# Optimization experiments

Hardware: AMD Instinct MI355X
Metric: run time of the kernel (lower is better)

## Reference

```python
import jax, jax.numpy as jnp
import numpy as np

E, H, V, B, T = 256, 512, 50257, 4, 512
EPS = 1e-5  # torch F.layer_norm default


def _ln(x):
    m = jnp.mean(x, axis=-1, keepdims=True)
    v = jnp.var(x, axis=-1, keepdims=True)
    return (x - m) / jnp.sqrt(v + EPS)


def setup_inputs() -> dict:
    key = jax.random.key(0)
    ks = iter(jax.random.split(key, 40))

    def w(shape):
        return jax.random.normal(next(ks), shape, dtype=jnp.float32) * 0.02

    inp = {"input_ids": jax.random.randint(next(ks), (B, T), 0, V)}
    inp["emb_table"] = w((V, E))
    for i, e in [(0, E), (1, H)]:  # layer 0 input = emb_dim, layer 1 input = hidden_dim
        inp[f"Wc1_{i}"] = w((2 * H + e, 2 * H)); inp[f"bc1_{i}"] = w((2 * H,))
        inp[f"Wc2_{i}"] = w((2 * H, H));         inp[f"bc2_{i}"] = w((H,))
        inp[f"Wg1_{i}"] = w((2 * H + e, H));     inp[f"bg1_{i}"] = w((H,))
        inp[f"Wg2_{i}"] = w((H, 1));             inp[f"bg2_{i}"] = w((1,))
        inp[f"Wr_{i}"] = w((e, H));              inp[f"br_{i}"] = w((H,))
    inp["Wa1"] = w((H, H)); inp["ba1"] = w((H,))
    inp["Wa2"] = w((H, 1)); inp["ba2"] = w((1,))
    inp["Wh"] = w((H, V));  inp["bh"] = w((V,))
    return inp


def _forward(input_ids, emb_table,
             Wc1_0, bc1_0, Wc2_0, bc2_0, Wg1_0, bg1_0, Wg2_0, bg2_0, Wr_0, br_0,
             Wc1_1, bc1_1, Wc2_1, bc2_1, Wg1_1, bg1_1, Wg2_1, bg2_1, Wr_1, br_1,
             Wa1, ba1, Wa2, ba2, Wh, bh):
    layers = [
        (Wc1_0, bc1_0, Wc2_0, bc2_0, Wg1_0, bg1_0, Wg2_0, bg2_0, Wr_0, br_0),
        (Wc1_1, bc1_1, Wc2_1, bc2_1, Wg1_1, bg1_1, Wg2_1, bg2_1, Wr_1, br_1),
    ]
    emb = emb_table[input_ids]  # [B,T,E]

    def step(carry, x_t):
        h2s, h1s = carry  # tuples of [B,H] per layer
        new_h2, new_h1 = [], []
        inp = x_t
        gate = None
        for (Wc1, bc1, Wc2, bc2, Wg1, bg1, Wg2, bg2, Wr, br), h2, h1 in zip(layers, h2s, h1s):
            ctx = jnp.concatenate([h1, h2, inp], axis=-1)  # [B, 2H+e]
            cand = jnp.maximum(ctx @ Wc1 + bc1, 0.0) @ Wc2 + bc2
            gate = jax.nn.sigmoid(jnp.tanh(ctx @ Wg1 + bg1) @ Wg2 + bg2)[:, 0]  # [B]
            h = _ln(h1 + gate[:, None] * cand + 0.1 * (inp @ Wr + br))
            new_h2.append(h1); new_h1.append(h)
            inp = h
        return (tuple(new_h2), tuple(new_h1)), (inp, gate)

    z = jnp.zeros((B, H), emb.dtype)
    init = ((z, z), (z, z))
    _, (hist, gates) = jax.lax.scan(step, init, jnp.swapaxes(emb, 0, 1))
    hist = jnp.swapaxes(hist, 0, 1)    # [B,T,H] last-layer hidden states
    gates = jnp.swapaxes(gates, 0, 1)  # [B,T]

    # Additive attention over the growing prefix: scores are fixed per position,
    # so prefix-softmax context = cumsum(exp(s)*h) / cumsum(exp(s)).
    scores = (jnp.tanh(hist @ Wa1 + ba1) @ Wa2 + ba2)[..., 0]  # [B,T]
    m = jnp.max(scores, axis=1, keepdims=True)
    e = jnp.exp(scores - m)
    num = jnp.cumsum(e[..., None] * hist, axis=1)  # [B,T,H]
    den = jnp.cumsum(e, axis=1)[..., None]
    attended = hist + num / den
    logits = attended @ Wh + bh  # [B,T,V]
    return logits, gates


def reference(input_ids, emb_table,
              Wc1_0, bc1_0, Wc2_0, bc2_0, Wg1_0, bg1_0, Wg2_0, bg2_0, Wr_0, br_0,
              Wc1_1, bc1_1, Wc2_1, bc2_1, Wg1_1, bg1_1, Wg2_1, bg2_1, Wr_1, br_1,
              Wa1, ba1, Wa2, ba2, Wh, bh):
    return _forward(input_ids, emb_table,
                    Wc1_0, bc1_0, Wc2_0, bc2_0, Wg1_0, bg1_0, Wg2_0, bg2_0, Wr_0, br_0,
                    Wc1_1, bc1_1, Wc2_1, bc2_1, Wg1_1, bg1_1, Wg2_1, bg2_1, Wr_1, br_1,
                    Wa1, ba1, Wa2, ba2, Wh, bh)
```

## Files before the change

### kernel.cpp

```cpp
#include <hip/hip_runtime.h>
#include <hip/hip_fp16.h>
#include <cstdint>
#include <cstddef>

typedef unsigned short u16;
typedef unsigned int   u32;
typedef unsigned long long u64;

#define Bn 4
#define Tn 512
#define Hn 512
#define En 256
#define Vn 50257
#define NPAD 50304
#define RG  256
#define RNT 256

typedef _Float16 h2t __attribute__((ext_vector_type(2)));

#if defined(__has_builtin)
#if __has_builtin(__builtin_amdgcn_fdot2)
#define HAS_FDOT2 1
#endif
#endif
__device__ __forceinline__ float fdot2f(h2t a, h2t b, float c) {
#ifdef HAS_FDOT2
  return __builtin_amdgcn_fdot2(a, b, c, false);
#else
  return fmaf((float)a[0], (float)b[0], fmaf((float)a[1], (float)b[1], c));
#endif
}

__device__ __forceinline__ u16 f2bf(float f) {
  u32 x; __builtin_memcpy(&x, &f, 4);
  u32 r = (x + 0x7fffu + ((x >> 16) & 1u)) >> 16;
  return (u16)r;
}
__device__ __forceinline__ u16 f2h(float f) {
  __half hh = __float2half(f); u16 u; __builtin_memcpy(&u, &hh, 2); return u;
}
__device__ __forceinline__ u64 gldu64(const u64* p) {
  return __hip_atomic_load(p, __ATOMIC_RELAXED, __HIP_MEMORY_SCOPE_AGENT);
}
__device__ __forceinline__ void gstu64(u64* p, u64 v) {
  __hip_atomic_store(p, v, __ATOMIC_RELAXED, __HIP_MEMORY_SCOPE_AGENT);
}
__device__ __forceinline__ u32 gldu32(const u32* p) {
  return __hip_atomic_load(p, __ATOMIC_RELAXED, __HIP_MEMORY_SCOPE_AGENT);
}
__device__ __forceinline__ void gstu32(u32* p, u32 v) {
  __hip_atomic_store(p, v, __ATOMIC_RELAXED, __HIP_MEMORY_SCOPE_AGENT);
}
__device__ __forceinline__ void gstf(float* p, float v) {
  __hip_atomic_store(p, v, __ATOMIC_RELAXED, __HIP_MEMORY_SCOPE_AGENT);
}

__global__ __launch_bounds__(256) void transpose_h(
    const float* __restrict__ src, __half* __restrict__ dst, int K, int N)
{
  __shared__ float tile[32][33];
  const int tx = threadIdx.x & 31, ty = threadIdx.x >> 5;
  const int bn = blockIdx.x * 32, bk = blockIdx.y * 32;
  #pragma unroll
  for (int i = 0; i < 4; ++i)
    tile[ty + i * 8][tx] = src[(size_t)(bk + ty + i * 8) * N + bn + tx];
  __syncthreads();
  #pragma unroll
  for (int i = 0; i < 4; ++i)
    dst[(size_t)(bn + ty + i * 8) * K + bk + tx] = __float2half(tile[tx][ty + i * 8]);
}

__global__ __launch_bounds__(256) void convwh_kernel(
    const float* __restrict__ wh, u16* __restrict__ whb)
{
  const int k = blockIdx.y;
  const int v0 = (blockIdx.x * 256 + threadIdx.x) * 2;
  if (v0 >= NPAD) return;
  float a = (v0     < Vn) ? wh[(size_t)k * Vn + v0]     : 0.f;
  float b = (v0 + 1 < Vn) ? wh[(size_t)k * Vn + v0 + 1] : 0.f;
  u32 pack = (u32)f2bf(a) | ((u32)f2bf(b) << 16);
  *(u32*)&whb[(size_t)k * NPAD + v0] = pack;
}

#define HR16_B  98304
#define HR0_B   102400
#define EMB_B   104448
#define XCAND_B 105472
#define GP_B    109568
#define RLOC_B  110080
#define SS_B    110144
#define BC1L_B  110464
#define BG1L_B  110528
#define BC2L_B  110560
#define BRL_B   110592
#define WG2L_B  110624
#define BG2L_B  110656
#define STW_B   110720
#define STW0_B  110784
#define REC_LDS 110848

__global__ __launch_bounds__(RNT, 1) void rec_kernel(
    const int* __restrict__ ids, const float* __restrict__ emb,
    const __half* wtC1_0, const __half* wtG1_0, const __half* wtC2_0, const __half* wtR_0,
    const __half* wtC1_1, const __half* wtG1_1, const __half* wtC2_1, const __half* wtR_1,
    const float* bc1_0, const float* bg1_0, const float* bc2_0, const float* br_0,
    const float* wg2_0, const float* bg2_0,
    const float* bc1_1, const float* bg1_1, const float* bc2_1, const float* br_1,
    const float* wg2_1, const float* bg2_1,
    u32* flagA, u64* HB, u64* CB,
    float* __restrict__ histN, float* __restrict__ gates_out)
{
  extern __shared__ char smem[];
  __half* WL    = (__half*)smem;
  __half* hr16  = (__half*)(smem + HR16_B);
  __half* hr0   = (__half*)(smem + HR0_B);
  __half* xcand = (__half*)(smem + XCAND_B);
  float* gp     = (float*)(smem + GP_B);
  float* rloc   = (float*)(smem + RLOC_B);
  float* Ss     = (float*)(smem + SS_B);
  float* bc1L   = (float*)(smem + BC1L_B);
  float* bg1L   = (float*)(smem + BG1L_B);
  float* bc2L   = (float*)(smem + BC2L_B);
  float* brL    = (float*)(smem + BRL_B);
  float* wg2L   = (float*)(smem + WG2L_B);
  float* bg2L   = (float*)(smem + BG2L_B);
  float* stw    = (float*)(smem + STW_B);
  float* stw0   = (float*)(smem + STW0_B);

  const int tid = threadIdx.x, g = blockIdx.x;
  const int bp = g >> 7, l = (g >> 6) & 1, gl = g & 63;
  const int w = tid >> 6, lane = tid & 63;
  const int C = l ? 1536 : 1280;
  const int e = l ? 512 : 256;
  const int oG1 = 16 * C, oR = 24 * C, oC2 = 24 * C + 8 * e;

  const __half* wtC1 = l ? wtC1_1 : wtC1_0;
  const __half* wtG1 = l ? wtG1_1 : wtG1_0;
  const __half* wtC2 = l ? wtC2_1 : wtC2_0;
  const __half* wtR  = l ? wtR_1  : wtR_0;
  const float* bc1 = l ? bc1_1 : bc1_0;
  const float* bg1 = l ? bg1_1 : bg1_0;
  const float* bc2 = l ? bc2_1 : bc2_0;
  const float* br  = l ? br_1  : br_0;
  const float* wg2 = l ? wg2_1 : wg2_0;
  const float* bg2 = l ? bg2_1 : bg2_0;

  u64* HBown = HB + (size_t)((bp * 2 + l) * 2) * 512;
  u64* CBown = CB + (size_t)((bp * 2 + l) * 2) * 1152;
  const u64* HBl0 = HB + (size_t)((bp * 2) * 2) * 512;

  {
    auto cp = [&](const __half* src, int nh, int offh) {
      const u32* s = (const u32*)src; u32* d = (u32*)(WL + offh);
      for (int i = tid; i < (nh >> 1); i += RNT) d[i] = s[i];
    };
    cp(wtC1 + (size_t)(gl * 16) * C, 16 * C, 0);
    cp(wtG1 + (size_t)(gl * 8) * C,  8 * C, oG1);
    cp(wtR  + (size_t)(gl * 8) * e,  8 * e, oR);
    cp(wtC2 + (size_t)(gl * 8) * 1024, 8 * 1024, oC2);
  }
  for (int i = tid; i < 2960; i += RNT) ((u32*)(smem + HR16_B))[i] = 0;
  __syncthreads();

  if (tid < 16)      bc1L[tid] = bc1[gl * 16 + tid];
  else if (tid < 24) bg1L[tid - 16] = bg1[gl * 8 + tid - 16];
  else if (tid < 32) bc2L[tid - 24] = bc2[gl * 8 + tid - 24];
  else if (tid < 40) brL[tid - 32]  = br[gl * 8 + tid - 32];
  else if (tid < 48) wg2L[tid - 40] = wg2[gl * 8 + tid - 40];
  else if (tid == 48) bg2L[0] = bg2[0];
  for (int task = w; task < 32; task += 4) {
    const __half* colp; int K;
    if (task < 16)      { colp = WL + (size_t)task * C;              K = C; }
    else if (task < 24) { colp = WL + oG1 + (size_t)(task - 16) * C; K = C; }
    else                { colp = WL + oR  + (size_t)(task - 24) * e; K = e; }
    float s1 = 0.f, s2 = 0.f, s3 = 0.f;
    for (int k = lane; k < K; k += 64) {
      float v = __half2float(colp[k]);
      if (K == e) s1 += v;
      else if (k < 512) s1 += v;
      else if (k < 1024) s2 += v;
      else s3 += v;
    }
    #pragma unroll
    for (int off = 32; off; off >>= 1) {
      s1 += __shfl_xor(s1, off); s2 += __shfl_xor(s2, off); s3 += __shfl_xor(s3, off);
    }
    if (lane == 0) {
      if (task < 16)      { Ss[task] = s1; Ss[16 + task] = s2; Ss[32 + task] = s3; }
      else if (task < 24) { Ss[48 + task - 16] = s1; Ss[56 + task - 16] = s2; Ss[64 + task - 16] = s3; }
      else                { Ss[72 + task - 24] = s1; }
    }
  }
  __syncthreads();

  const int nEnd = l ? (Tn + 1) : (Tn - 1);
  float mp[2] = {0.f, 0.f}, ipv[2] = {0.f, 0.f};

  for (int n = 0; n <= nEnd; ++n) {
    const int t = n - l;
    const bool prod = (t >= 0) && (t < Tn);
    const bool pollOwn = (t >= 1) && (t <= Tn);
    const bool pollL0  = (l == 1) && prod;
    const int parR = (n - 1) & 1;

    h2t er0[2], er1[2];
    er0[0] = (h2t)0; er0[1] = (h2t)0; er1[0] = (h2t)0; er1[1] = (h2t)0;
    if (l == 0 && prod) {
      int id0 = ids[(bp * 2) * Tn + t];
      int id1 = ids[(bp * 2 + 1) * Tn + t];
      float2 fa0 = *(const float2*)(emb + (size_t)id0 * En + 2 * lane);
      float2 fb0 = *(const float2*)(emb + (size_t)id0 * En + 2 * (lane + 64));
      float2 fa1 = *(const float2*)(emb + (size_t)id1 * En + 2 * lane);
      float2 fb1 = *(const float2*)(emb + (size_t)id1 * En + 2 * (lane + 64));
      er0[0][0] = (_Float16)fa0.x; er0[0][1] = (_Float16)fa0.y;
      er0[1][0] = (_Float16)fb0.x; er0[1][1] = (_Float16)fb0.y;
      er1[0][0] = (_Float16)fa1.x; er1[0][1] = (_Float16)fa1.y;
      er1[1][0] = (_Float16)fb1.x; er1[1][1] = (_Float16)fb1.y;
    }

    float comb[8][2];
    #pragma unroll
    for (int c = 0; c < 8; ++c) { comb[c][0] = 0.f; comb[c][1] = 0.f; }
    if (prod) {
      const __half* h2pl[2] = { hr16 + ((parR ^ 1) * 2) * 512,
                                hr16 + ((parR ^ 1) * 2 + 1) * 512 };
      float a[8][2];
      if (w < 3) {
        const __half* wbase = (w < 2) ? (WL + (size_t)(w * 8) * C) : (WL + oG1);
        #pragma unroll
        for (int c = 0; c < 8; ++c) { a[c][0] = 0.f; a[c][1] = 0.f; }
        #pragma unroll
        for (int it = 0; it < 4; ++it) {
          int p2 = lane + it * 64;
          h2t x0 = *(const h2t*)(h2pl[0] + 2 * p2);
          h2t x1 = *(const h2t*)(h2pl[1] + 2 * p2);
          #pragma unroll
          for (int c = 0; c < 8; ++c) {
            h2t wv = *(const h2t*)(wbase + (size_t)c * C + 512 + 2 * p2);
            a[c][0] = fdot2f(wv, x0, a[c][0]);
            a[c][1] = fdot2f(wv, x1, a[c][1]);
          }
        }
        #pragma unroll
        for (int c = 0; c < 8; ++c) { comb[c][0] += ipv[0] * a[c][0]; comb[c][1] += ipv[1] * a[c][1]; }
        if (l == 0) {
          #pragma unroll
          for (int c = 0; c < 8; ++c) { a[c][0] = 0.f; a[c][1] = 0.f; }
          #pragma unroll
          for (int it = 0; it < 2; ++it) {
            int p2 = lane + it * 64;
            #pragma unroll
            for (int c = 0; c < 8; ++c) {
              h2t wv = *(const h2t*)(wbase + (size_t)c * C + 1024 + 2 * p2);
              a[c][0] = fdot2f(wv, er0[it], a[c][0]);
              a[c][1] = fdot2f(wv, er1[it], a[c][1]);
            }
          }
          #pragma unroll
          for (int c = 0; c < 8; ++c) { comb[c][0] += a[c][0]; comb[c][1] += a[c][1]; }
        }
      } else if (l == 0) {
        #pragma unroll
        for (int c = 0; c < 8; ++c) { a[c][0] = 0.f; a[c][1] = 0.f; }
        #pragma unroll
        for (int it = 0; it < 2; ++it) {
          int p2 = lane + it * 64;
          #pragma unroll
          for (int c = 0; c < 8; ++c) {
            h2t wv = *(const h2t*)(WL + oR + (size_t)c * e + 2 * p2);
            a[c][0] = fdot2f(wv, er0[it], a[c][0]);
            a[c][1] = fdot2f(wv, er1[it], a[c][1]);
          }
        }
        #pragma unroll
        for (int c = 0; c < 8; ++c) { comb[c][0] = a[c][0]; comb[c][1] = a[c][1]; }
      }
    }

    if (pollOwn || pollL0) {
      const u64* s1 = HBown + (size_t)parR * 512;
      const u64* s0 = HBl0 + (size_t)parR * 512;
      const u32 want = (u32)n;
      u64 v1[2], v0[2];
      for (;;) {
        bool ok = true;
        if (pollOwn) { v1[0] = gldu64(s1 + tid); v1[1] = gldu64(s1 + 256 + tid); }
        if (pollL0)  { v0[0] = gldu64(s0 + tid); v0[1] = gldu64(s0 + 256 + tid); }
        if (pollOwn) ok &= ((u32)(v1[0] >> 32) == want) & ((u32)(v1[1] >> 32) == want);
        if (pollL0)  ok &= ((u32)(v0[0] >> 32) == want) & ((u32)(v0[1] >> 32) == want);
        if (ok) break;
        __builtin_amdgcn_s_sleep(2);
      }
      if (pollOwn) {
        float sb0 = 0.f, sb1 = 0.f, qb0 = 0.f, qb1 = 0.f;
        #pragma unroll
        for (int i = 0; i < 2; ++i) {
          int W = i * 256 + tid;
          int glp = W >> 3, q = W & 7, cpp = q >> 1, b = q & 1;
          u32 pay = (u32)v1[i];
          ((u32*)(hr16 + (parR * 2 + b) * 512))[glp * 4 + cpp] = pay;
          __half2 hh; __builtin_memcpy(&hh, &pay, 4);
          float2 fv = __half22float2(hh);
          float sv = fv.x + fv.y, qv = fv.x * fv.x + fv.y * fv.y;
          if (b == 0) { sb0 += sv; qb0 += qv; } else { sb1 += sv; qb1 += qv; }
        }
        #pragma unroll
        for (int off = 32; off; off >>= 1) {
          sb0 += __shfl_xor(sb0, off); qb0 += __shfl_xor(qb0, off);
          sb1 += __shfl_xor(sb1, off); qb1 += __shfl_xor(qb1, off);
        }
        if (lane == 0) { stw[w * 4] = sb0; stw[w * 4 + 1] = sb1; stw[w * 4 + 2] = qb0; stw[w * 4 + 3] = qb1; }
      }
      if (pollL0) {
        float sb0 = 0.f, sb1 = 0.f, qb0 = 0.f, qb1 = 0.f;
        #pragma unroll
        for (int i = 0; i < 2; ++i) {
          int W = i * 256 + tid;
          int glp = W >> 3, q = W & 7, cpp = q >> 1, b = q & 1;
          u32 pay = (u32)v0[i];
          ((u32*)(hr0 + b * 512))[glp * 4 + cpp] = pay;
          __half2 hh; __builtin_memcpy(&hh, &pay, 4);
          float2 fv = __half22float2(hh);
          float sv = fv.x + fv.y, qv = fv.x * fv.x + fv.y * fv.y;
          if (b == 0) { sb0 += sv; qb0 += qv; } else { sb1 += sv; qb1 += qv; }
        }
        #pragma unroll
        for (int off = 32; off; off >>= 1) {
          sb0 += __shfl_xor(sb0, off); qb0 += __shfl_xor(qb0, off);
          sb1 += __shfl_xor(sb1, off); qb1 += __shfl_xor(qb1, off);
        }
        if (lane == 0) { stw0[w * 4] = sb0; stw0[w * 4 + 1] = sb1; stw0[w * 4 + 2] = qb0; stw0[w * 4 + 3] = qb1; }
      }
    }
    __syncthreads();
    if (l == 1 && tid == 0) gstu32(flagA + (bp * 64 + gl) * 16, (u32)(n + 1));

    float m1[2] = {0.f, 0.f}, i1v[2] = {0.f, 0.f};
    float m3[2] = {0.f, 0.f}, i3v[2] = {0.f, 0.f};
    if (pollOwn) {
      float S0 = stw[0] + stw[4] + stw[8] + stw[12];
      float S1 = stw[1] + stw[5] + stw[9] + stw[13];
      float Q0 = stw[2] + stw[6] + stw[10] + stw[14];
      float Q1 = stw[3] + stw[7] + stw[11] + stw[15];
      m1[0] = S0 * (1.f / 512.f); i1v[0] = rsqrtf(Q0 * (1.f / 512.f) - m1[0] * m1[0] + 1e-5f);
      m1[1] = S1 * (1.f / 512.f); i1v[1] = rsqrtf(Q1 * (1.f / 512.f) - m1[1] * m1[1] + 1e-5f);
    }
    if (pollL0) {
      float S0 = stw0[0] + stw0[4] + stw0[8] + stw0[12];
      float S1 = stw0[1] + stw0[5] + stw0[9] + stw0[13];
      float Q0 = stw0[2] + stw0[6] + stw0[10] + stw0[14];
      float Q1 = stw0[3] + stw0[7] + stw0[11] + stw0[15];
      m3[0] = S0 * (1.f / 512.f); i3v[0] = rsqrtf(Q0 * (1.f / 512.f) - m3[0] * m3[0] + 1e-5f);
      m3[1] = S1 * (1.f / 512.f); i3v[1] = rsqrtf(Q1 * (1.f / 512.f) - m3[1] * m3[1] + 1e-5f);
    }

    if (l == 1 && pollOwn && tid < 16) {
      int c = tid >> 1, b = tid & 1, j = gl * 8 + c;
      float rv = __half2float(hr16[(parR * 2 + b) * 512 + j]);
      gstf(histN + ((size_t)((bp * 2 + b) * Tn + (t - 1))) * Hn + j, (rv - m1[b]) * i1v[b]);
    }

    if (prod) {
      const __half* h1pl[2] = { hr16 + (parR * 2) * 512, hr16 + (parR * 2 + 1) * 512 };
      float a[8][2];
      if (w < 3) {
        const __half* wbase = (w < 2) ? (WL + (size_t)(w * 8) * C) : (WL + oG1);
        #pragma unroll
        for (int c = 0; c < 8; ++c) { a[c][0] = 0.f; a[c][1] = 0.f; }
        #pragma unroll
        for (int it = 0; it < 4; ++it) {
          int p2 = lane + it * 64;
          h2t x0 = *(const h2t*)(h1pl[0] + 2 * p2);
          h2t x1 = *(const h2t*)(h1pl[1] + 2 * p2);
          #pragma unroll
          for (int c = 0; c < 8; ++c) {
            h2t wv = *(const h2t*)(wbase + (size_t)c * C + 2 * p2);
            a[c][0] = fdot2f(wv, x0, a[c][0]);
            a[c][1] = fdot2f(wv, x1, a[c][1]);
          }
        }
        #pragma unroll
        for (int c = 0; c < 8; ++c) { comb[c][0] += i1v[0] * a[c][0]; comb[c][1] += i1v[1] * a[c][1]; }
        if (l == 1) {
          #pragma unroll
          for (int c = 0; c < 8; ++c) { a[c][0] = 0.f; a[c][1] = 0.f; }
          #pragma unroll
          for (int it = 0; it < 4; ++it) {
            int p2 = lane + it * 64;
            h2t x0 = *(const h2t*)(hr0 + 2 * p2);
            h2t x1 = *(const h2t*)(hr0 + 512 + 2 * p2);
            #pragma unroll
            for (int c = 0; c < 8; ++c) {
              h2t wv = *(const h2t*)(wbase + (size_t)c * C + 1024 + 2 * p2);
              a[c][0] = fdot2f(wv, x0, a[c][0]);
              a[c][1] = fdot2f(wv, x1, a[c][1]);
            }
          }
          #pragma unroll
          for (int c = 0; c < 8; ++c) { comb[c][0] += i3v[0] * a[c][0]; comb[c][1] += i3v[1] * a[c][1]; }
        }
      } else if (l == 1) {
        #pragma unroll
        for (int c = 0; c < 8; ++c) { a[c][0] = 0.f; a[c][1] = 0.f; }
        #pragma unroll
        for (int it = 0; it < 4; ++it) {
          int p2 = lane + it * 64;
          h2t x0 = *(const h2t*)(hr0 + 2 * p2);
          h2t x1 = *(const h2t*)(hr0 + 512 + 2 * p2);
          #pragma unroll
          for (int c = 0; c < 8; ++c) {
            h2t wv = *(const h2t*)(WL + oR + (size_t)c * e + 2 * p2);
            a[c][0] = fdot2f(wv, x0, a[c][0]);
            a[c][1] = fdot2f(wv, x1, a[c][1]);
          }
        }
        #pragma unroll
        for (int c = 0; c < 8; ++c) { comb[c][0] = i3v[0] * a[c][0]; comb[c][1] = i3v[1] * a[c][1]; }
      }

      #pragma unroll
      for (int off = 32; off; off >>= 1)
        #pragma unroll
        for (int c = 0; c < 8; ++c) {
          comb[c][0] += __shfl_xor(comb[c][0], off);
          comb[c][1] += __shfl_xor(comb[c][1], off);
        }
      float v0s = 0.f, v1s = 0.f;
      #pragma unroll
      for (int c = 0; c < 8; ++c)
        if (lane == c) { v0s = comb[c][0]; v1s = comb[c][1]; }

      const u64 tagw = ((u64)(u32)(n + 1)) << 32;
      u64* CBw = CBown + (size_t)(n & 1) * 1152 + gl * 18;
      if (w < 2) {
        if (lane < 8) {
          int cg = w * 8 + lane;
          float k0 = i1v[0] * m1[0] * Ss[cg] + ipv[0] * mp[0] * Ss[16 + cg];
          float k1 = i1v[1] * m1[1] * Ss[cg] + ipv[1] * mp[1] * Ss[16 + cg];
          if (l) { k0 += i3v[0] * m3[0] * Ss[32 + cg]; k1 += i3v[1] * m3[1] * Ss[32 + cg]; }
          float bb = bc1L[cg];
          float c0 = fmaxf(v0s - k0 + bb, 0.f), c1 = fmaxf(v1s - k1 + bb, 0.f);
          u32 pay = (u32)f2h(c0) | ((u32)f2h(c1) << 16);
          gstu64(CBw + cg, tagw | pay);
        }
      } else if (w == 2) {
        if (lane < 8) {
          float k0 = i1v[0] * m1[0] * Ss[48 + lane] + ipv[0] * mp[0] * Ss[56 + lane];
          float k1 = i1v[1] * m1[1] * Ss[48 + lane] + ipv[1] * mp[1] * Ss[56 + lane];
          if (l) { k0 += i3v[0] * m3[0] * Ss[64 + lane]; k1 += i3v[1] * m3[1] * Ss[64 + lane]; }
          float bgv = bg1L[lane], wgv = wg2L[lane];
          float t0 = tanhf(v0s - k0 + bgv) * wgv;
          float t1 = tanhf(v1s - k1 + bgv) * wgv;
          #pragma unroll
          for (int off = 1; off < 8; off <<= 1) { t0 += __shfl_xor(t0, off); t1 += __shfl_xor(t1, off); }
          if (lane == 0) {
            u32 b0, b1; __builtin_memcpy(&b0, &t0, 4); __builtin_memcpy(&b1, &t1, 4);
            gstu64(CBw + 16, tagw | b0);
            gstu64(CBw + 17, tagw | b1);
          }
        }
      } else {
        if (lane < 8) {
          float k0 = l ? i3v[0] * m3[0] * Ss[72 + lane] : 0.f;
          float k1 = l ? i3v[1] * m3[1] * Ss[72 + lane] : 0.f;
          rloc[lane * 2]     = v0s - k0 + brL[lane];
          rloc[lane * 2 + 1] = v1s - k1 + brL[lane];
        }
      }
    }

    if (prod) {
      const u64* CBL = CBown + (size_t)(n & 1) * 1152;
      const u32 want = (u32)(n + 1);
      const bool needF = (l == 0) && (tid < 64);
      const u32* fptr = flagA + (bp * 64 + tid) * 16;
      u64 cv[5];
      const bool last = (tid < 128);
      for (;;) {
        bool ok = true;
        #pragma unroll
        for (int i = 0; i < 4; ++i) cv[i] = gldu64(CBL + i * 256 + tid);
        if (last) cv[4] = gldu64(CBL + 1024 + tid);
        #pragma unroll
        for (int i = 0; i < 4; ++i) ok &= ((u32)(cv[i] >> 32) == want);
        if (last) ok &= ((u32)(cv[4] >> 32) == want);
        if (needF) ok &= (gldu32(fptr) >= (u32)n);
        if (ok) break;
        __builtin_amdgcn_s_sleep(2);
      }
      u16* xc16 = (u16*)xcand;
      #pragma unroll
      for (int i = 0; i < 5; ++i) {
        if (i == 4 && !last) break;
        int idx = i * 256 + tid;
        int p = (int)(((u32)idx * 3641u) >> 16);
        int w2 = idx - p * 18;
        u32 pay = (u32)cv[i];
        if (w2 < 16) {
          int j = p * 16 + w2;
          xc16[j]        = (u16)(pay & 0xffffu);
          xc16[1024 + j] = (u16)(pay >> 16);
        } else {
          float f; __builtin_memcpy(&f, &pay, 4);
          gp[p * 2 + (w2 - 16)] = f;
        }
      }
    }
    __syncthreads();

    if (prod) {
      float gs0 = gp[lane * 2], gs1 = gp[lane * 2 + 1];
      #pragma unroll
      for (int off = 32; off; off >>= 1) { gs0 += __shfl_xor(gs0, off); gs1 += __shfl_xor(gs1, off); }
      float gate[2];
      gate[0] = 1.f / (1.f + expf(-(gs0 + bg2L[0])));
      gate[1] = 1.f / (1.f + expf(-(gs1 + bg2L[0])));

      float a2[2][2];
      a2[0][0] = a2[0][1] = a2[1][0] = a2[1][1] = 0.f;
      const __half* wb2 = WL + oC2 + (w * 2) * 1024;
      #pragma unroll
      for (int it = 0; it < 8; ++it) {
        int p2 = lane + it * 64;
        h2t xv0 = *(const h2t*)(xcand + 2 * p2);
        h2t xv1 = *(const h2t*)(xcand + 1024 + 2 * p2);
        #pragma unroll
        for (int cc = 0; cc < 2; ++cc) {
          h2t wv = *(const h2t*)(wb2 + cc * 1024 + 2 * p2);
          a2[cc][0] = fdot2f(wv, xv0, a2[cc][0]);
          a2[cc][1] = fdot2f(wv, xv1, a2[cc][1]);
        }
      }
      #pragma unroll
      for (int off = 32; off; off >>= 1)
        #pragma unroll
        for (int cc = 0; cc < 2; ++cc) {
          a2[cc][0] += __shfl_xor(a2[cc][0], off);
          a2[cc][1] += __shfl_xor(a2[cc][1], off);
        }
      float sel = 0.f;
      #pragma unroll
      for (int cc = 0; cc < 2; ++cc)
        #pragma unroll
        for (int b = 0; b < 2; ++b)
          if (lane == cc * 2 + b) sel = a2[cc][b];
      int cc = (lane >> 1) & 1, b = lane & 1, cl = w * 2 + cc;
      float rv = __half2float(hr16[(parR * 2 + b) * 512 + gl * 8 + cl]);
      float h1n = (rv - m1[b]) * i1v[b];
      float hv = h1n + gate[b] * (sel + bc2L[cl]) + 0.1f * rloc[cl * 2 + b];
      float hv0 = __shfl(hv, 0), hv1 = __shfl(hv, 1);
      float hv2 = __shfl(hv, 2), hv3 = __shfl(hv, 3);
      if (lane < 2) {
        u32 pay = (lane == 0) ? ((u32)f2h(hv0) | ((u32)f2h(hv2) << 16))
                              : ((u32)f2h(hv1) | ((u32)f2h(hv3) << 16));
        u64* HBw = HBown + (size_t)(n & 1) * 512 + gl * 8;
        gstu64(HBw + w * 2 + lane, (((u64)(u32)(n + 1)) << 32) | pay);
      }
      if (l == 1 && gl == 0 && w == 0 && lane == 0) {
        gstf(gates_out + (bp * 2) * Tn + t, gate[0]);
        gstf(gates_out + (bp * 2 + 1) * Tn + t, gate[1]);
      }
    }

    if (pollOwn) { mp[0] = m1[0]; mp[1] = m1[1]; ipv[0] = i1v[0]; ipv[1] = i1v[1]; }
  }
}

__global__ __launch_bounds__(256) void scores_kernel(
    const float* __restrict__ histN,
    const float* __restrict__ wa1, const float* __restrict__ ba1,
    const float* __restrict__ wa2, const float* __restrict__ ba2,
    float* __restrict__ scores)
{
  __shared__ float xs[8][512];
  __shared__ float wacc[4][8];
  const int tid = threadIdx.x, bid = blockIdx.x;

  for (int idx = tid; idx < 4096; idx += 256)
    xs[idx >> 9][idx & 511] = histN[(size_t)(bid * 8) * Hn + idx];
  __syncthreads();

  float pr[8] = {0.f,0.f,0.f,0.f,0.f,0.f,0.f,0.f};
  #pragma unroll
  for (int cc = 0; cc < 2; ++cc) {
    int c = tid + cc * 256;
    float a[8] = {0.f,0.f,0.f,0.f,0.f,0.f,0.f,0.f};
    for (int k = 0; k < 512; ++k) {
      float wv = wa1[(size_t)k * 512 + c];
      #pragma unroll
      for (int r = 0; r < 8; ++r) a[r] = fmaf(xs[r][k], wv, a[r]);
    }
    float b1 = ba1[c], w2 = wa2[c];
    #pragma unroll
    for (int r = 0; r < 8; ++r) pr[r] += tanhf(a[r] + b1) * w2;
  }
  int lane = tid & 63, wq = tid >> 6;
  #pragma unroll
  for (int off = 32; off; off >>= 1)
    #pragma unroll
    for (int r = 0; r < 8; ++r) pr[r] += __shfl_xor(pr[r], off);
  if (lane == 0) {
    #pragma unroll
    for (int r = 0; r < 8; ++r) wacc[wq][r] = pr[r];
  }
  __syncthreads();
  if (tid < 8)
    scores[bid * 8 + tid] = wacc[0][tid] + wacc[1][tid] + wacc[2][tid] + wacc[3][tid] + ba2[0];
}

__global__ __launch_bounds__(256) void cumsum_scan_kernel(
    const float* __restrict__ scores, const float* __restrict__ histN,
    u16* __restrict__ att)
{
  __shared__ float ee[512], sa[512], sb[512], red[256];
  __shared__ float tile[64][64];
  const int tid = threadIdx.x;
  const int b = blockIdx.y, j0 = blockIdx.x * 64;

  float s0 = scores[b * Tn + tid], s1 = scores[b * Tn + tid + 256];
  red[tid] = fmaxf(s0, s1);
  __syncthreads();
  for (int s = 128; s; s >>= 1) { if (tid < s) red[tid] = fmaxf(red[tid], red[tid + s]); __syncthreads(); }
  float m = red[0];
  ee[tid] = expf(s0 - m); ee[tid + 256] = expf(s1 - m);
  sa[tid] = ee[tid]; sa[tid + 256] = ee[tid + 256];
  __syncthreads();
  float* A = sa; float* D = sb;
  for (int off = 1; off < 512; off <<= 1) {
    for (int t2 = tid; t2 < 512; t2 += 256) { float v = A[t2]; if (t2 >= off) v += A[t2 - off]; D[t2] = v; }
    __syncthreads();
    float* tmp = A; A = D; D = tmp;
  }
  float* R = D;
  for (int t2 = tid; t2 < 512; t2 += 256) R[t2] = 1.f / A[t2];
  __syncthreads();

  float ax = 0.f;
  for (int tt = 0; tt < 8; ++tt) {
    #pragma unroll
    for (int k = 0; k < 16; ++k) {
      int idx = tid + k * 256;
      int r = idx >> 6, c = idx & 63;
      tile[r][c] = histN[(size_t)(b * Tn + tt * 64 + r) * Hn + j0 + c];
    }
    __syncthreads();
    if (tid < 64) {
      for (int r = 0; r < 64; ++r) {
        int t = tt * 64 + r;
        float x = tile[r][tid];
        ax = fmaf(ee[t], x, ax);
        att[((size_t)(b * Tn + t)) * Hn + j0 + tid] = f2bf(x + ax * R[t]);
      }
    }
    __syncthreads();
  }
}

typedef short bf16x8_t __attribute__((ext_vector_type(8)));
typedef float f32x4_t  __attribute__((ext_vector_type(4)));

__global__ __launch_bounds__(256) void gemm_kernel(
    const u16* __restrict__ Aw, const u16* __restrict__ Bw,
    const float* __restrict__ bh, float* __restrict__ out)
{
  __shared__ u16 Alds[128 * 64];
  __shared__ u16 Blds[64 * 128];
  const int tid = threadIdx.x;
  const int n0 = blockIdx.x * 128, m0 = blockIdx.y * 128;
  const int w = tid >> 6, lane = tid & 63;
  const int wm = (w & 1) * 64, wn = (w >> 1) * 64;

  f32x4_t acc[4][4];
  #pragma unroll
  for (int i = 0; i < 4; ++i)
    #pragma unroll
    for (int j = 0; j < 4; ++j) acc[i][j] = (f32x4_t){0.f, 0.f, 0.f, 0.f};

  for (int kt = 0; kt < 8; ++kt) {
    const int k0 = kt * 64;
    {
      int row = tid >> 1, kc = (tid & 1) * 32;
      #pragma unroll
      for (int jj = 0; jj < 4; ++jj) {
        uint4 v = *(const uint4*)(Aw + (size_t)(m0 + row) * 512 + k0 + kc + jj * 8);
        int byte = row * 128 + (kc + jj * 8) * 2;
        byte ^= (row & 7) << 4;
        *(uint4*)((char*)Alds + byte) = v;
      }
    }
    {
      #pragma unroll
      for (int q = 0; q < 4; ++q) {
        int r = (tid >> 4) + q * 16, c8 = (tid & 15) * 8;
        uint4 v = *(const uint4*)(Bw + (size_t)(k0 + r) * NPAD + n0 + c8);
        *(uint4*)&Blds[r * 128 + c8] = v;
      }
    }
    __syncthreads();
    #pragma unroll
    for (int kh = 0; kh < 2; ++kh) {
      bf16x8_t af[4];
      #pragma unroll
      for (int i = 0; i < 4; ++i) {
        int row = wm + i * 16 + (lane & 15);
        int byte = row * 128 + kh * 64 + (lane >> 4) * 16;
        byte ^= (row & 7) << 4;
        af[i] = *(const bf16x8_t*)((const char*)Alds + byte);
      }
      const int kb = kh * 32 + (lane >> 4) * 8;
      #pragma unroll
      for (int j = 0; j < 4; ++j) {
        int col = wn + j * 16 + (lane & 15);
        bf16x8_t bf;
        #pragma unroll
        for (int jj = 0; jj < 8; ++jj) bf[jj] = (short)Blds[(kb + jj) * 128 + col];
        #pragma unroll
        for (int i = 0; i < 4; ++i)
          acc[i][j] = __builtin_amdgcn_mfma_f32_16x16x32_bf16(af[i], bf, acc[i][j], 0, 0, 0);
      }
    }
    __syncthreads();
  }
  #pragma unroll
  for (int j = 0; j < 4; ++j) {
    int col = n0 + wn + j * 16 + (lane & 15);
    if (col < Vn) {
      float bias = bh[col];
      #pragma unroll
      for (int i = 0; i < 4; ++i) {
        int rbase = m0 + wm + i * 16 + (lane >> 4) * 4;
        #pragma unroll
        for (int r = 0; r < 4; ++r)
          out[(size_t)(rbase + r) * Vn + col] = acc[i][j][r] + bias;
      }
    }
  }
}

extern "C" void kernel_launch(void* const* d_in, const int* in_sizes, int n_in,
                              void* d_out, int out_size, void* d_ws, size_t ws_size,
                              hipStream_t stream) {
  const int*   ids  = (const int*)d_in[0];
  const float* emb  = (const float*)d_in[1];
  const float* Wc1_0 = (const float*)d_in[2];  const float* bc1_0 = (const float*)d_in[3];
  const float* Wc2_0 = (const float*)d_in[4];  const float* bc2_0 = (const float*)d_in[5];
  const float* Wg1_0 = (const float*)d_in[6];  const float* bg1_0 = (const float*)d_in[7];
  const float* Wg2_0 = (const float*)d_in[8];  const float* bg2_0 = (const float*)d_in[9];
  const float* Wr_0  = (const float*)d_in[10]; const float* br_0  = (const float*)d_in[11];
  const float* Wc1_1 = (const float*)d_in[12]; const float* bc1_1 = (const float*)d_in[13];
  const float* Wc2_1 = (const float*)d_in[14]; const float* bc2_1 = (const float*)d_in[15];
  const float* Wg1_1 = (const float*)d_in[16]; const float* bg1_1 = (const float*)d_in[17];
  const float* Wg2_1 = (const float*)d_in[18]; const float* bg2_1 = (const float*)d_in[19];
  const float* Wr_1  = (const float*)d_in[20]; const float* br_1  = (const float*)d_in[21];
  const float* Wa1 = (const float*)d_in[22]; const float* ba1 = (const float*)d_in[23];
  const float* Wa2 = (const float*)d_in[24]; const float* ba2 = (const float*)d_in[25];
  const float* Wh  = (const float*)d_in[26]; const float* bh  = (const float*)d_in[27];

  float* out = (float*)d_out;
  char*  ws  = (char*)d_ws;

  const size_t OFF_FLAGA = 0;
  const size_t OFF_HB    = 8192;
  const size_t OFF_CB    = 40960;
  const size_t OFF_WT    = 114688;
  const size_t OFF_HISTN = OFF_WT + 11534336;
  const size_t OFF_SCO   = OFF_HISTN + 4194304;
  const size_t OFF_ATT   = OFF_SCO + 8192;
  const size_t OFF_WHB   = OFF_ATT + 2097152;

  u32*   flagA  = (u32*)(ws + OFF_FLAGA);
  u64*   HB     = (u64*)(ws + OFF_HB);
  u64*   CB     = (u64*)(ws + OFF_CB);
  __half* wth   = (__half*)(ws + OFF_WT);
  float* histN  = (float*)(ws + OFF_HISTN);
  float* scores = (float*)(ws + OFF_SCO);
  u16*   att    = (u16*)(ws + OFF_ATT);
  u16*   whb    = (u16*)(ws + OFF_WHB);
  float* gates  = out + (size_t)Bn * Tn * Vn;

  __half* wtC1_0h = wth;
  __half* wtG1_0h = wth + 1310720;
  __half* wtC2_0h = wth + 1966080;
  __half* wtR_0h  = wth + 2490368;
  __half* wtC1_1h = wth + 2621440;
  __half* wtG1_1h = wth + 4194304;
  __half* wtC2_1h = wth + 4980736;
  __half* wtR_1h  = wth + 5505024;

  hipMemsetAsync(ws, 0, 114688, stream);

  transpose_h<<<dim3(32, 40), 256, 0, stream>>>(Wc1_0, wtC1_0h, 1280, 1024);
  transpose_h<<<dim3(16, 40), 256, 0, stream>>>(Wg1_0, wtG1_0h, 1280, 512);
  transpose_h<<<dim3(16, 32), 256, 0, stream>>>(Wc2_0, wtC2_0h, 1024, 512);
  transpose_h<<<dim3(16,  8), 256, 0, stream>>>(Wr_0,  wtR_0h,   256, 512);
  transpose_h<<<dim3(32, 48), 256, 0, stream>>>(Wc1_1, wtC1_1h, 1536, 1024);
  transpose_h<<<dim3(16, 48), 256, 0, stream>>>(Wg1_1, wtG1_1h, 1536, 512);
  transpose_h<<<dim3(16, 32), 256, 0, stream>>>(Wc2_1, wtC2_1h, 1024, 512);
  transpose_h<<<dim3(16, 16), 256, 0, stream>>>(Wr_1,  wtR_1h,   512, 512);

  convwh_kernel<<<dim3(99, 512), 256, 0, stream>>>(Wh, whb);

  (void)hipFuncSetAttribute((const void*)rec_kernel,
                            hipFuncAttributeMaxDynamicSharedMemorySize, REC_LDS);

  rec_kernel<<<dim3(RG), dim3(RNT), REC_LDS, stream>>>(
      ids, emb,
      wtC1_0h, wtG1_0h, wtC2_0h, wtR_0h,
      wtC1_1h, wtG1_1h, wtC2_1h, wtR_1h,
      bc1_0, bg1_0, bc2_0, br_0, Wg2_0, bg2_0,
      bc1_1, bg1_1, bc2_1, br_1, Wg2_1, bg2_1,
      flagA, HB, CB, histN, gates);

  scores_kernel<<<dim3(256), 256, 0, stream>>>(histN, Wa1, ba1, Wa2, ba2, scores);

  cumsum_scan_kernel<<<dim3(8, Bn), 256, 0, stream>>>(scores, histN, att);

  gemm_kernel<<<dim3(393, 16), 256, 0, stream>>>(att, whb, bh, out);
}
```

Baseline: 4.331 ms.

## Split polling so layer-1 consumes layer-0 input before waiting on own recurrence

The combined wait for the block's own previous hidden state and layer 0's new output is split into two phases. Layer-1 blocks now poll only for the layer-0 output first, publish their flag, and compute the matvec contributions that depend on it (the input part of the context, plus the residual projection). Only after that do they wait for their own recurrent state and finish the h1 part. This moves work ahead of the longer recurrence dependency to shorten each step's critical path, at the cost of an extra __syncthreads and a reordered comb accumulation that has to stay consistent (the l==0 path now uses += instead of =).

```diff
diff --git a/kernel.cpp b/kernel.cpp
--- a/kernel.cpp
+++ b/kernel.cpp
@@ -273,45 +273,21 @@
           }
         }
         #pragma unroll
-        for (int c = 0; c < 8; ++c) { comb[c][0] = a[c][0]; comb[c][1] = a[c][1]; }
-      }
-    }
-
-    if (pollOwn || pollL0) {
-      const u64* s1 = HBown + (size_t)parR * 512;
-      const u64* s0 = HBl0 + (size_t)parR * 512;
-      const u32 want = (u32)n;
-      u64 v1[2], v0[2];
-      for (;;) {
-        bool ok = true;
-        if (pollOwn) { v1[0] = gldu64(s1 + tid); v1[1] = gldu64(s1 + 256 + tid); }
-        if (pollL0)  { v0[0] = gldu64(s0 + tid); v0[1] = gldu64(s0 + 256 + tid); }
-        if (pollOwn) ok &= ((u32)(v1[0] >> 32) == want) & ((u32)(v1[1] >> 32) == want);
-        if (pollL0)  ok &= ((u32)(v0[0] >> 32) == want) & ((u32)(v0[1] >> 32) == want);
-        if (ok) break;
-        __builtin_amdgcn_s_sleep(2);
-      }
-      if (pollOwn) {
-        float sb0 = 0.f, sb1 = 0.f, qb0 = 0.f, qb1 = 0.f;
-        #pragma unroll
-        for (int i = 0; i < 2; ++i) {
-          int W = i * 256 + tid;
-          int glp = W >> 3, q = W & 7, cpp = q >> 1, b = q & 1;
-          u32 pay = (u32)v1[i];
-          ((u32*)(hr16 + (parR * 2 + b) * 512))[glp * 4 + cpp] = pay;
-          __half2 hh; __builtin_memcpy(&hh, &pay, 4);
-          float2 fv = __half22float2(hh);
-          float sv = fv.x + fv.y, qv = fv.x * fv.x + fv.y * fv.y;
-          if (b == 0) { sb0 += sv; qb0 += qv; } else { sb1 += sv; qb1 += qv; }
-        }
-        #pragma unroll
-        for (int off = 32; off; off >>= 1) {
-          sb0 += __shfl_xor(sb0, off); qb0 += __shfl_xor(qb0, off);
-          sb1 += __shfl_xor(sb1, off); qb1 += __shfl_xor(qb1, off);
-        }
-        if (lane == 0) { stw[w * 4] = sb0; stw[w * 4 + 1] = sb1; stw[w * 4 + 2] = qb0; stw[w * 4 + 3] = qb1; }
-      }
+        for (int c = 0; c < 8; ++c) { comb[c][0] += a[c][0]; comb[c][1] += a[c][1]; }
+      }
+    }
+
+    float m3[2] = {0.f, 0.f}, i3v[2] = {0.f, 0.f};
+    if (l == 1) {
       if (pollL0) {
+        const u64* s0 = HBl0 + (size_t)parR * 512;
+        const u32 want = (u32)n;
+        u64 v0[2];
+        for (;;) {
+          v0[0] = gldu64(s0 + tid); v0[1] = gldu64(s0 + 256 + tid);
+          if (((u32)(v0[0] >> 32) == want) & ((u32)(v0[1] >> 32) == want)) break;
+          __builtin_amdgcn_s_sleep(2);
+        }
         float sb0 = 0.f, sb1 = 0.f, qb0 = 0.f, qb1 = 0.f;
         #pragma unroll
         for (int i = 0; i < 2; ++i) {
@@ -331,59 +307,22 @@
         }
         if (lane == 0) { stw0[w * 4] = sb0; stw0[w * 4 + 1] = sb1; stw0[w * 4 + 2] = qb0; stw0[w * 4 + 3] = qb1; }
       }
-    }
-    __syncthreads();
-    if (l == 1 && tid == 0) gstu32(flagA + (bp * 64 + gl) * 16, (u32)(n + 1));
-
-    float m1[2] = {0.f, 0.f}, i1v[2] = {0.f, 0.f};
-    float m3[2] = {0.f, 0.f}, i3v[2] = {0.f, 0.f};
-    if (pollOwn) {
-      float S0 = stw[0] + stw[4] + stw[8] + stw[12];
-      float S1 = stw[1] + stw[5] + stw[9] + stw[13];
-      float Q0 = stw[2] + stw[6] + stw[10] + stw[14];
-      float Q1 = stw[3] + stw[7] + stw[11] + stw[15];
-      m1[0] = S0 * (1.f / 512.f); i1v[0] = rsqrtf(Q0 * (1.f / 512.f) - m1[0] * m1[0] + 1e-5f);
-      m1[1] = S1 * (1.f / 512.f); i1v[1] = rsqrtf(Q1 * (1.f / 512.f) - m1[1] * m1[1] + 1e-5f);
-    }
-    if (pollL0) {
-      float S0 = stw0[0] + stw0[4] + stw0[8] + stw0[12];
-      float S1 = stw0[1] + stw0[5] + stw0[9] + stw0[13];
-      float Q0 = stw0[2] + stw0[6] + stw0[10] + stw0[14];
-      float Q1 = stw0[3] + stw0[7] + stw0[11] + stw0[15];
-      m3[0] = S0 * (1.f / 512.f); i3v[0] = rsqrtf(Q0 * (1.f / 512.f) - m3[0] * m3[0] + 1e-5f);
-      m3[1] = S1 * (1.f / 512.f); i3v[1] = rsqrtf(Q1 * (1.f / 512.f) - m3[1] * m3[1] + 1e-5f);
-    }
-
-    if (l == 1 && pollOwn && tid < 16) {
-      int c = tid >> 1, b = tid & 1, j = gl * 8 + c;
-      float rv = __half2float(hr16[(parR * 2 + b) * 512 + j]);
-      gstf(histN + ((size_t)((bp * 2 + b) * Tn + (t - 1))) * Hn + j, (rv - m1[b]) * i1v[b]);
-    }
-
-    if (prod) {
-      const __half* h1pl[2] = { hr16 + (parR * 2) * 512, hr16 + (parR * 2 + 1) * 512 };
-      float a[8][2];
-      if (w < 3) {
-        const __half* wbase = (w < 2) ? (WL + (size_t)(w * 8) * C) : (WL + oG1);
+      __syncthreads();
+      if (tid == 0) gstu32(flagA + (bp * 64 + gl) * 16, (u32)(n + 1));
+      if (pollL0) {
+        {
+          float S0 = stw0[0] + stw0[4] + stw0[8] + stw0[12];
+          float S1 = stw0[1] + stw0[5] + stw0[9] + stw0[13];
+          float Q0 = stw0[2] + stw0[6] + stw0[10] + stw0[14];
+          float Q1 = stw0[3] + stw0[7] + stw0[11] + stw0[15];
+          m3[0] = S0 * (1.f / 512.f); i3v[0] = rsqrtf(Q0 * (1.f / 512.f) - m3[0] * m3[0] + 1e-5f);
+          m3[1] = S1 * (1.f / 512.f); i3v[1] = rsqrtf(Q1 * (1.f / 512.f) - m3[1] * m3[1] + 1e-5f);
+        }
+        float a[8][2];
         #pragma unroll
         for (int c = 0; c < 8; ++c) { a[c][0] = 0.f; a[c][1] = 0.f; }
-        #pragma unroll
-        for (int it = 0; it < 4; ++it) {
-          int p2 = lane + it * 64;
-          h2t x0 = *(const h2t*)(h1pl[0] + 2 * p2);
-          h2t x1 = *(const h2t*)(h1pl[1] + 2 * p2);
-          #pragma unroll
-          for (int c = 0; c < 8; ++c) {
-            h2t wv = *(const h2t*)(wbase + (size_t)c * C + 2 * p2);
-            a[c][0] = fdot2f(wv, x0, a[c][0]);
-            a[c][1] = fdot2f(wv, x1, a[c][1]);
-          }
-        }
-        #pragma unroll
-        for (int c = 0; c < 8; ++c) { comb[c][0] += i1v[0] * a[c][0]; comb[c][1] += i1v[1] * a[c][1]; }
-        if (l == 1) {
-          #pragma unroll
-          for (int c = 0; c < 8; ++c) { a[c][0] = 0.f; a[c][1] = 0.f; }
+        if (w < 3) {
+          const __half* wbase = (w < 2) ? (WL + (size_t)(w * 8) * C) : (WL + oG1);
           #pragma unroll
           for (int it = 0; it < 4; ++it) {
             int p2 = lane + it * 64;
@@ -396,26 +335,92 @@
               a[c][1] = fdot2f(wv, x1, a[c][1]);
             }
           }
+        } else {
           #pragma unroll
-          for (int c = 0; c < 8; ++c) { comb[c][0] += i3v[0] * a[c][0]; comb[c][1] += i3v[1] * a[c][1]; }
-        }
-      } else if (l == 1) {
+          for (int it = 0; it < 4; ++it) {
+            int p2 = lane + it * 64;
+            h2t x0 = *(const h2t*)(hr0 + 2 * p2);
+            h2t x1 = *(const h2t*)(hr0 + 512 + 2 * p2);
+            #pragma unroll
+            for (int c = 0; c < 8; ++c) {
+              h2t wv = *(const h2t*)(WL + oR + (size_t)c * e + 2 * p2);
+              a[c][0] = fdot2f(wv, x0, a[c][0]);
+              a[c][1] = fdot2f(wv, x1, a[c][1]);
+            }
+          }
+        }
+        #pragma unroll
+        for (int c = 0; c < 8; ++c) { comb[c][0] += i3v[0] * a[c][0]; comb[c][1] += i3v[1] * a[c][1]; }
+      }
+    }
+
+    if (pollOwn) {
+      const u64* s1 = HBown + (size_t)parR * 512;
+      const u32 want = (u32)n;
+      u64 v1[2];
+      for (;;) {
+        v1[0] = gldu64(s1 + tid); v1[1] = gldu64(s1 + 256 + tid);
+        if (((u32)(v1[0] >> 32) == want) & ((u32)(v1[1] >> 32) == want)) break;
+        __builtin_amdgcn_s_sleep(2);
+      }
+      float sb0 = 0.f, sb1 = 0.f, qb0 = 0.f, qb1 = 0.f;
+      #pragma unroll
+      for (int i = 0; i < 2; ++i) {
+        int W = i * 256 + tid;
+        int glp = W >> 3, q = W & 7, cpp = q >> 1, b = q & 1;
+        u32 pay = (u32)v1[i];
+        ((u32*)(hr16 + (parR * 2 + b) * 512))[glp * 4 + cpp] = pay;
+        __half2 hh; __builtin_memcpy(&hh, &pay, 4);
+        float2 fv = __half22float2(hh);
+        float sv = fv.x + fv.y, qv = fv.x * fv.x + fv.y * fv.y;
+        if (b == 0) { sb0 += sv; qb0 += qv; } else { sb1 += sv; qb1 += qv; }
+      }
+      #pragma unroll
+      for (int off = 32; off; off >>= 1) {
+        sb0 += __shfl_xor(sb0, off); qb0 += __shfl_xor(qb0, off);
+        sb1 += __shfl_xor(sb1, off); qb1 += __shfl_xor(qb1, off);
+      }
+      if (lane == 0) { stw[w * 4] = sb0; stw[w * 4 + 1] = sb1; stw[w * 4 + 2] = qb0; stw[w * 4 + 3] = qb1; }
+    }
+    __syncthreads();
+
+    float m1[2] = {0.f, 0.f}, i1v[2] = {0.f, 0.f};
+    if (pollOwn) {
+      float S0 = stw[0] + stw[4] + stw[8] + stw[12];
+      float S1 = stw[1] + stw[5] + stw[9] + stw[13];
+      float Q0 = stw[2] + stw[6] + stw[10] + stw[14];
+      float Q1 = stw[3] + stw[7] + stw[11] + stw[15];
+      m1[0] = S0 * (1.f / 512.f); i1v[0] = rsqrtf(Q0 * (1.f / 512.f) - m1[0] * m1[0] + 1e-5f);
+      m1[1] = S1 * (1.f / 512.f); i1v[1] = rsqrtf(Q1 * (1.f / 512.f) - m1[1] * m1[1] + 1e-5f);
+    }
+
+    if (l == 1 && pollOwn && tid < 16) {
+      int c = tid >> 1, b = tid & 1, j = gl * 8 + c;
+      float rv = __half2float(hr16[(parR * 2 + b) * 512 + j]);
+      gstf(histN + ((size_t)((bp * 2 + b) * Tn + (t - 1))) * Hn + j, (rv - m1[b]) * i1v[b]);
+    }
+
+    if (prod) {
+      const __half* h1pl[2] = { hr16 + (parR * 2) * 512, hr16 + (parR * 2 + 1) * 512 };
+      if (w < 3) {
+        const __half* wbase = (w < 2) ? (WL + (size_t)(w * 8) * C) : (WL + oG1);
+        float a[8][2];
         #pragma unroll
         for (int c = 0; c < 8; ++c) { a[c][0] = 0.f; a[c][1] = 0.f; }
         #pragma unroll
         for (int it = 0; it < 4; ++it) {
           int p2 = lane + it * 64;
-          h2t x0 = *(const h2t*)(hr0 + 2 * p2);
-          h2t x1 = *(const h2t*)(hr0 + 512 + 2 * p2);
+          h2t x0 = *(const h2t*)(h1pl[0] + 2 * p2);
+          h2t x1 = *(const h2t*)(h1pl[1] + 2 * p2);
           #pragma unroll
           for (int c = 0; c < 8; ++c) {
-            h2t wv = *(const h2t*)(WL + oR + (size_t)c * e + 2 * p2);
+            h2t wv = *(const h2t*)(wbase + (size_t)c * C + 2 * p2);
             a[c][0] = fdot2f(wv, x0, a[c][0]);
             a[c][1] = fdot2f(wv, x1, a[c][1]);
           }
         }
         #pragma unroll
-        for (int c = 0; c < 8; ++c) { comb[c][0] = i3v[0] * a[c][0]; comb[c][1] = i3v[1] * a[c][1]; }
+        for (int c = 0; c < 8; ++c) { comb[c][0] += i1v[0] * a[c][0]; comb[c][1] += i1v[1] * a[c][1]; }
       }
 
       #pragma unroll
```

Measured after the change: 4.227 ms. 1.02x faster.
